# Optimization experiments

Measured on AMD Instinct MI355X. Metric: run time of the kernel, lower is better.

The kernel has to match this reference:

```python
import jax, jax.numpy as jnp
import numpy as np

ORDER = 2


def _masked_row_mean(v, m, safe_cnt, has_any):
    # v already zeroed outside mask; per-row mean over masked entries
    s = jnp.sum(v, axis=1, keepdims=True) / safe_cnt
    return jnp.where(has_any, s, 0.0)


def high_order_residual(x, mask, order=ORDER):
    """Vectorized faithful version of high_order_residual (braq).
    nanmean over masked entries == masked sum / count; sign/scale/shift
    are only meaningful inside the mask, outputs outside the mask are 0.
    """
    m = mask.astype(x.dtype)                       # (oc, ic)
    cnt = jnp.sum(m, axis=1, keepdims=True)        # (oc, 1)
    safe_cnt = jnp.maximum(cnt, 1.0)
    has_any = cnt > 0
    xm = x * m
    sum_order = jnp.zeros_like(x)
    for _ in range(order):
        residual = (xm - sum_order) * m            # masked residual, 0 outside
        mean = _masked_row_mean(residual, m, safe_cnt, has_any)   # (oc,1)
        centered = (residual - mean) * m           # 0 outside mask
        scale = _masked_row_mean(jnp.abs(centered), m, safe_cnt, has_any)
        binary = jnp.sign(centered) * scale + mean
        sum_order = sum_order + binary * m
    return sum_order


def setup_inputs() -> dict:
    key = jax.random.key(0)
    k1, k2 = jax.random.split(key)
    x = jax.random.normal(k1, (11008, 4096), dtype=jnp.float32) * 0.02
    mask = jax.random.randint(k2, (11008, 4096), 0, 2).astype(jnp.bool_)
    return {"x": x, "mask": mask}


def reference(x, mask):
    return high_order_residual(x, mask, ORDER)
```

## Files before the change

### kernel.cpp

```cpp
#include <hip/hip_runtime.h>
#include <stdint.h>

#define IC   4096
#define BLK  256
#define VPT  4
#define EPT  (VPT * 4)

__device__ __forceinline__ void block_red_df(double& a, float& b, double* smd, float* smf) {
    #pragma unroll
    for (int off = 32; off; off >>= 1) {
        a += __shfl_xor(a, off);
        b += __shfl_xor(b, off);
    }
    const int wid = threadIdx.x >> 6;
    if ((threadIdx.x & 63) == 0) { smd[wid] = a; smf[wid] = b; }
    __syncthreads();
    a = smd[0] + smd[1] + smd[2] + smd[3];
    b = smf[0] + smf[1] + smf[2] + smf[3];
}

__device__ __forceinline__ double block_red_d(double a, double* smd) {
    #pragma unroll
    for (int off = 32; off; off >>= 1) a += __shfl_xor(a, off);
    const int wid = threadIdx.x >> 6;
    if ((threadIdx.x & 63) == 0) smd[wid] = a;
    __syncthreads();
    return smd[0] + smd[1] + smd[2] + smd[3];
}

__global__ __launch_bounds__(BLK) void binarize_kernel(
    const float* __restrict__ x,
    const uint8_t* __restrict__ mask,
    float* __restrict__ out)
{
    __shared__ double smd[12];
    __shared__ float  smf[8];
    __shared__ int    smi[4];
    const int row = blockIdx.x;
    const int tid = threadIdx.x;

    int bad = (((const uint32_t*)mask)[tid] > 1u) ? 1 : 0;
    bad = __any(bad);
    if ((tid & 63) == 0) smi[tid >> 6] = bad;
    __syncthreads();
    const bool mask_is_i32 = ((smi[0] | smi[1] | smi[2] | smi[3]) == 0);

    const float* xr   = x + (size_t)row * IC;
    float*       orow = out + (size_t)row * IC;

    float xm[EPT];
    float sgm[EPT];
    uint32_t mb = 0;

    #pragma unroll
    for (int i = 0; i < VPT; ++i) {
        float4 v = ((const float4*)xr)[tid + i * BLK];
        xm[i*4+0] = v.x; xm[i*4+1] = v.y; xm[i*4+2] = v.z; xm[i*4+3] = v.w;
    }

    if (mask_is_i32) {
        const int4* mr = (const int4*)mask + (size_t)row * (IC / 4);
        #pragma unroll
        for (int i = 0; i < VPT; ++i) {
            int4 m4 = mr[tid + i * BLK];
            mb |= (uint32_t)(m4.x != 0) << (i*4+0);
            mb |= (uint32_t)(m4.y != 0) << (i*4+1);
            mb |= (uint32_t)(m4.z != 0) << (i*4+2);
            mb |= (uint32_t)(m4.w != 0) << (i*4+3);
        }
    } else {
        const uint32_t* mr = (const uint32_t*)(mask + (size_t)row * IC);
        #pragma unroll
        for (int i = 0; i < VPT; ++i) {
            uint32_t w = mr[tid + i * BLK];
            mb |= (uint32_t)((w & 0x000000ffu) != 0) << (i*4+0);
            mb |= (uint32_t)((w & 0x0000ff00u) != 0) << (i*4+1);
            mb |= (uint32_t)((w & 0x00ff0000u) != 0) << (i*4+2);
            mb |= (uint32_t)((w & 0xff000000u) != 0) << (i*4+3);
        }
    }

    #pragma unroll
    for (int j = 0; j < EPT; ++j)
        xm[j] = ((mb >> j) & 1u) ? xm[j] : 0.f;

    double sA[2] = {0.0, 0.0};
    #pragma unroll
    for (int j = 0; j < EPT; ++j) sA[j & 1] += (double)xm[j];
    double s  = sA[0] + sA[1];
    float  cf = (float)__popc(mb);
    block_red_df(s, cf, smd + 0, smf + 0);

    const bool   has   = (cf > 0.f);
    const double c     = (double)cf;
    const double nmiss = (double)(4096.f - cf);
    const double inv   = 1.0 / fmax(c, 1.0);
    const double mean1 = has ? s * inv : 0.0;
    const float  mean1f = (float)mean1;

    double saB[2] = {0.0, 0.0};
    float  dB[2]  = {0.f, 0.f};
    #pragma unroll
    for (int j = 0; j < EPT; ++j) {
        const float t  = xm[j] - mean1f;
        const float sg = (t > 0.f) ? 1.f : ((t < 0.f) ? -1.f : 0.f);
        const float smv = ((mb >> j) & 1u) ? sg : 0.f;
        sgm[j] = smv;
        dB[j & 1]  += smv;
        saB[j & 1] += (double)fabsf(t);
    }
    double sa = saB[0] + saB[1];
    float  df = dB[0] + dB[1];
    block_red_df(sa, df, smd + 4, smf + 4);
    sa -= nmiss * (double)fabsf(mean1f);

    const double scale1 = has ? sa * inv : 0.0;
    const double mean2  = has ? (s - scale1 * (double)df - mean1 * c) * inv : 0.0;
    const double mean12 = mean1 + mean2;

    double sbD[2] = {0.0, 0.0};
    #pragma unroll
    for (int j = 0; j < EPT; ++j) {
        const double t2 = (double)xm[j] - fma((double)sgm[j], scale1, mean12);
        sgm[j] = (float)t2;
        sbD[j & 1] += fabs(t2);
    }
    double sa2 = block_red_d(sbD[0] + sbD[1], smd + 8);
    sa2 -= nmiss * fabs(mean12);
    const double scale2 = has ? sa2 * inv : 0.0;
    const float  scale2f = (float)scale2;

    #pragma unroll
    for (int i = 0; i < VPT; ++i) {
        float r[4];
        #pragma unroll
        for (int k = 0; k < 4; ++k) {
            const int j = i * 4 + k;
            const float t2f = sgm[j];
            const float b1f = xm[j] - t2f;
            const float sg2 = (t2f > 0.f) ? 1.f : ((t2f < 0.f) ? -1.f : 0.f);
            const float o   = fmaf(sg2, scale2f, b1f);
            r[k] = ((mb >> j) & 1u) ? o : 0.f;
        }
        float4 o; o.x = r[0]; o.y = r[1]; o.z = r[2]; o.w = r[3];
        ((float4*)orow)[tid + i * BLK] = o;
    }
}

extern "C" void kernel_launch(void* const* d_in, const int* in_sizes, int n_in,
                              void* d_out, int out_size, void* d_ws, size_t ws_size,
                              hipStream_t stream) {
    const float*   x    = (const float*)d_in[0];
    const uint8_t* mask = (const uint8_t*)d_in[1];
    float*         out  = (float*)d_out;

    const int rows = in_sizes[0] / IC;
    binarize_kernel<<<rows, BLK, 0, stream>>>(x, mask, out);
}
```

Before: 402.6 us.

## Process one row per wavefront with shuffle-only reductions, recomputing signs

Switches from one 256-thread block per row to one 64-lane wavefront per row (4 rows per block), so row reductions use only wave shuffles and need no shared memory or __syncthreads. Each lane now holds 64 elements, and the per-element sign array is dropped and recomputed in later passes to save registers. The trade-off is more registers per lane, possibly lower occupancy, extra recomputation in double precision, and a longer serial load chain per lane.

```diff
diff --git a/kernel.cpp b/kernel.cpp
--- a/kernel.cpp
+++ b/kernel.cpp
@@ -1,149 +1,148 @@
 #include <hip/hip_runtime.h>
 #include <stdint.h>
 
-#define IC   4096
-#define BLK  256
-#define VPT  4
-#define EPT  (VPT * 4)
-
-__device__ __forceinline__ void block_red_df(double& a, float& b, double* smd, float* smf) {
-    #pragma unroll
-    for (int off = 32; off; off >>= 1) {
-        a += __shfl_xor(a, off);
-        b += __shfl_xor(b, off);
-    }
-    const int wid = threadIdx.x >> 6;
-    if ((threadIdx.x & 63) == 0) { smd[wid] = a; smf[wid] = b; }
-    __syncthreads();
-    a = smd[0] + smd[1] + smd[2] + smd[3];
-    b = smf[0] + smf[1] + smf[2] + smf[3];
-}
-
-__device__ __forceinline__ double block_red_d(double a, double* smd) {
-    #pragma unroll
-    for (int off = 32; off; off >>= 1) a += __shfl_xor(a, off);
-    const int wid = threadIdx.x >> 6;
-    if ((threadIdx.x & 63) == 0) smd[wid] = a;
-    __syncthreads();
-    return smd[0] + smd[1] + smd[2] + smd[3];
-}
+#define IC      4096
+#define BLK     256
+#define RPB     4
+#define CHUNKS  16
+#define EPT     64
 
 __global__ __launch_bounds__(BLK) void binarize_kernel(
     const float* __restrict__ x,
     const uint8_t* __restrict__ mask,
-    float* __restrict__ out)
+    float* __restrict__ out,
+    int nrows)
 {
-    __shared__ double smd[12];
-    __shared__ float  smf[8];
-    __shared__ int    smi[4];
-    const int row = blockIdx.x;
-    const int tid = threadIdx.x;
+    const int lane = threadIdx.x & 63;
+    const int row  = blockIdx.x * RPB + (threadIdx.x >> 6);
+    if (row >= nrows) return;
 
-    int bad = (((const uint32_t*)mask)[tid] > 1u) ? 1 : 0;
-    bad = __any(bad);
-    if ((tid & 63) == 0) smi[tid >> 6] = bad;
-    __syncthreads();
-    const bool mask_is_i32 = ((smi[0] | smi[1] | smi[2] | smi[3]) == 0);
+    const bool mask_is_i32 = !__any(((const uint32_t*)mask)[lane] > 1u);
 
-    const float* xr   = x + (size_t)row * IC;
+    const float* xr   = x   + (size_t)row * IC;
     float*       orow = out + (size_t)row * IC;
 
     float xm[EPT];
-    float sgm[EPT];
-    uint32_t mb = 0;
-
     #pragma unroll
-    for (int i = 0; i < VPT; ++i) {
-        float4 v = ((const float4*)xr)[tid + i * BLK];
-        xm[i*4+0] = v.x; xm[i*4+1] = v.y; xm[i*4+2] = v.z; xm[i*4+3] = v.w;
+    for (int i = 0; i < CHUNKS; ++i) {
+        float4 v = ((const float4*)xr)[lane + 64 * i];
+        xm[4*i+0] = v.x; xm[4*i+1] = v.y; xm[4*i+2] = v.z; xm[4*i+3] = v.w;
     }
 
+    uint32_t mw0 = 0, mw1 = 0;
     if (mask_is_i32) {
         const int4* mr = (const int4*)mask + (size_t)row * (IC / 4);
         #pragma unroll
-        for (int i = 0; i < VPT; ++i) {
-            int4 m4 = mr[tid + i * BLK];
-            mb |= (uint32_t)(m4.x != 0) << (i*4+0);
-            mb |= (uint32_t)(m4.y != 0) << (i*4+1);
-            mb |= (uint32_t)(m4.z != 0) << (i*4+2);
-            mb |= (uint32_t)(m4.w != 0) << (i*4+3);
+        for (int i = 0; i < CHUNKS; ++i) {
+            int4 m4 = mr[lane + 64 * i];
+            uint32_t b = (uint32_t)(m4.x != 0)
+                       | ((uint32_t)(m4.y != 0) << 1)
+                       | ((uint32_t)(m4.z != 0) << 2)
+                       | ((uint32_t)(m4.w != 0) << 3);
+            if (i < 8) mw0 |= b << (4 * i);
+            else       mw1 |= b << (4 * (i - 8));
         }
     } else {
         const uint32_t* mr = (const uint32_t*)(mask + (size_t)row * IC);
         #pragma unroll
-        for (int i = 0; i < VPT; ++i) {
-            uint32_t w = mr[tid + i * BLK];
-            mb |= (uint32_t)((w & 0x000000ffu) != 0) << (i*4+0);
-            mb |= (uint32_t)((w & 0x0000ff00u) != 0) << (i*4+1);
-            mb |= (uint32_t)((w & 0x00ff0000u) != 0) << (i*4+2);
-            mb |= (uint32_t)((w & 0xff000000u) != 0) << (i*4+3);
+        for (int i = 0; i < CHUNKS; ++i) {
+            uint32_t w = mr[lane + 64 * i];
+            uint32_t b = (uint32_t)((w & 0x000000ffu) != 0)
+                       | ((uint32_t)((w & 0x0000ff00u) != 0) << 1)
+                       | ((uint32_t)((w & 0x00ff0000u) != 0) << 2)
+                       | ((uint32_t)((w & 0xff000000u) != 0) << 3);
+            if (i < 8) mw0 |= b << (4 * i);
+            else       mw1 |= b << (4 * (i - 8));
         }
     }
 
     #pragma unroll
-    for (int j = 0; j < EPT; ++j)
-        xm[j] = ((mb >> j) & 1u) ? xm[j] : 0.f;
+    for (int j = 0; j < EPT; ++j) {
+        const uint32_t bit = ((j < 32 ? mw0 : mw1) >> (j & 31)) & 1u;
+        xm[j] = bit ? xm[j] : 0.f;
+    }
 
-    double sA[2] = {0.0, 0.0};
+    double sA0 = 0.0, sA1 = 0.0;
     #pragma unroll
-    for (int j = 0; j < EPT; ++j) sA[j & 1] += (double)xm[j];
-    double s  = sA[0] + sA[1];
-    float  cf = (float)__popc(mb);
-    block_red_df(s, cf, smd + 0, smf + 0);
+    for (int j = 0; j < EPT; j += 2) {
+        sA0 += (double)xm[j];
+        sA1 += (double)xm[j + 1];
+    }
+    double s  = sA0 + sA1;
+    float  cf = (float)(__popc(mw0) + __popc(mw1));
+    #pragma unroll
+    for (int off = 32; off; off >>= 1) {
+        s  += __shfl_xor(s,  off);
+        cf += __shfl_xor(cf, off);
+    }
 
-    const bool   has   = (cf > 0.f);
-    const double c     = (double)cf;
-    const double nmiss = (double)(4096.f - cf);
-    const double inv   = 1.0 / fmax(c, 1.0);
-    const double mean1 = has ? s * inv : 0.0;
+    const bool   has    = (cf > 0.f);
+    const double c      = (double)cf;
+    const double nmiss  = (double)(4096.f - cf);
+    const double inv    = 1.0 / fmax(c, 1.0);
+    const double mean1  = has ? s * inv : 0.0;
     const float  mean1f = (float)mean1;
 
-    double saB[2] = {0.0, 0.0};
-    float  dB[2]  = {0.f, 0.f};
+    double saB0 = 0.0, saB1 = 0.0;
+    float  dB0 = 0.f, dB1 = 0.f;
     #pragma unroll
     for (int j = 0; j < EPT; ++j) {
-        const float t  = xm[j] - mean1f;
-        const float sg = (t > 0.f) ? 1.f : ((t < 0.f) ? -1.f : 0.f);
-        const float smv = ((mb >> j) & 1u) ? sg : 0.f;
-        sgm[j] = smv;
-        dB[j & 1]  += smv;
-        saB[j & 1] += (double)fabsf(t);
+        const uint32_t bit = ((j < 32 ? mw0 : mw1) >> (j & 31)) & 1u;
+        const float t   = xm[j] - mean1f;
+        const float sg  = (t > 0.f) ? 1.f : ((t < 0.f) ? -1.f : 0.f);
+        const float smv = bit ? sg : 0.f;
+        if (j & 1) { dB1 += smv; saB1 += (double)fabsf(t); }
+        else       { dB0 += smv; saB0 += (double)fabsf(t); }
     }
-    double sa = saB[0] + saB[1];
-    float  df = dB[0] + dB[1];
-    block_red_df(sa, df, smd + 4, smf + 4);
+    double sa = saB0 + saB1;
+    float  df = dB0 + dB1;
+    #pragma unroll
+    for (int off = 32; off; off >>= 1) {
+        sa += __shfl_xor(sa, off);
+        df += __shfl_xor(df, off);
+    }
     sa -= nmiss * (double)fabsf(mean1f);
 
     const double scale1 = has ? sa * inv : 0.0;
     const double mean2  = has ? (s - scale1 * (double)df - mean1 * c) * inv : 0.0;
     const double mean12 = mean1 + mean2;
 
-    double sbD[2] = {0.0, 0.0};
+    double sb0 = 0.0, sb1 = 0.0;
     #pragma unroll
     for (int j = 0; j < EPT; ++j) {
-        const double t2 = (double)xm[j] - fma((double)sgm[j], scale1, mean12);
-        sgm[j] = (float)t2;
-        sbD[j & 1] += fabs(t2);
+        const uint32_t bit = ((j < 32 ? mw0 : mw1) >> (j & 31)) & 1u;
+        const float t   = xm[j] - mean1f;
+        const float sg  = (t > 0.f) ? 1.f : ((t < 0.f) ? -1.f : 0.f);
+        const float smv = bit ? sg : 0.f;
+        const double t2 = (double)xm[j] - fma((double)smv, scale1, mean12);
+        if (j & 1) sb1 += fabs(t2); else sb0 += fabs(t2);
     }
-    double sa2 = block_red_d(sbD[0] + sbD[1], smd + 8);
+    double sa2 = sb0 + sb1;
+    #pragma unroll
+    for (int off = 32; off; off >>= 1) sa2 += __shfl_xor(sa2, off);
     sa2 -= nmiss * fabs(mean12);
-    const double scale2 = has ? sa2 * inv : 0.0;
+    const double scale2  = has ? sa2 * inv : 0.0;
     const float  scale2f = (float)scale2;
 
     #pragma unroll
-    for (int i = 0; i < VPT; ++i) {
+    for (int i = 0; i < CHUNKS; ++i) {
         float r[4];
         #pragma unroll
         for (int k = 0; k < 4; ++k) {
-            const int j = i * 4 + k;
-            const float t2f = sgm[j];
+            const int j = 4 * i + k;
+            const uint32_t bit = ((j < 32 ? mw0 : mw1) >> (j & 31)) & 1u;
+            const float t   = xm[j] - mean1f;
+            const float sg  = (t > 0.f) ? 1.f : ((t < 0.f) ? -1.f : 0.f);
+            const float smv = bit ? sg : 0.f;
+            const double t2 = (double)xm[j] - fma((double)smv, scale1, mean12);
+            const float t2f = (float)t2;
             const float b1f = xm[j] - t2f;
             const float sg2 = (t2f > 0.f) ? 1.f : ((t2f < 0.f) ? -1.f : 0.f);
             const float o   = fmaf(sg2, scale2f, b1f);
-            r[k] = ((mb >> j) & 1u) ? o : 0.f;
+            r[k] = bit ? o : 0.f;
         }
-        float4 o; o.x = r[0]; o.y = r[1]; o.z = r[2]; o.w = r[3];
-        ((float4*)orow)[tid + i * BLK] = o;
+        float4 o4; o4.x = r[0]; o4.y = r[1]; o4.z = r[2]; o4.w = r[3];
+        ((float4*)orow)[lane + 64 * i] = o4;
     }
 }
 
@@ -155,5 +154,6 @@
     float*         out  = (float*)d_out;
 
     const int rows = in_sizes[0] / IC;
-    binarize_kernel<<<rows, BLK, 0, stream>>>(x, mask, out);
+    const int grid = (rows + RPB - 1) / RPB;
+    binarize_kernel<<<grid, BLK, 0, stream>>>(x, mask, out, rows);
 }
```

Measured after the change: 418.1 us. 3.9% more time.

## Process two rows per block and batch their block reductions together

Applied to the files above, without the earlier changes.

Each 256-thread block now handles two rows, interleaving their loads and sharing each shuffle/LDS reduction across both rows, so the number of barriers per row is halved. The per-element sign buffer is dropped and signs are recomputed from x and mean in later passes to save registers. The mask-format probe now uses a single wavefront instead of a shared-memory vote. In exchange, register pressure roughly doubles and the grid is halved, which may lower occupancy on a memory-bound kernel.

```diff
diff --git a/kernel.cpp b/kernel.cpp
--- a/kernel.cpp
+++ b/kernel.cpp
@@ -4,146 +4,200 @@
 #define IC   4096
 #define BLK  256
 #define VPT  4
-#define EPT  (VPT * 4)
-
-__device__ __forceinline__ void block_red_df(double& a, float& b, double* smd, float* smf) {
+#define EPT  16
+
+__device__ __forceinline__ void bred_2d2f(double& a, double& b, float& p, float& q,
+                                          double* smd, float* smf) {
     #pragma unroll
     for (int off = 32; off; off >>= 1) {
         a += __shfl_xor(a, off);
         b += __shfl_xor(b, off);
+        p += __shfl_xor(p, off);
+        q += __shfl_xor(q, off);
     }
     const int wid = threadIdx.x >> 6;
-    if ((threadIdx.x & 63) == 0) { smd[wid] = a; smf[wid] = b; }
+    if ((threadIdx.x & 63) == 0) { smd[wid] = a; smd[4 + wid] = b; smf[wid] = p; smf[4 + wid] = q; }
     __syncthreads();
-    a = smd[0] + smd[1] + smd[2] + smd[3];
-    b = smf[0] + smf[1] + smf[2] + smf[3];
-}
-
-__device__ __forceinline__ double block_red_d(double a, double* smd) {
-    #pragma unroll
-    for (int off = 32; off; off >>= 1) a += __shfl_xor(a, off);
+    a = (smd[0] + smd[1]) + (smd[2] + smd[3]);
+    b = (smd[4] + smd[5]) + (smd[6] + smd[7]);
+    p = (smf[0] + smf[1]) + (smf[2] + smf[3]);
+    q = (smf[4] + smf[5]) + (smf[6] + smf[7]);
+}
+
+__device__ __forceinline__ void bred_2d(double& a, double& b, double* smd) {
+    #pragma unroll
+    for (int off = 32; off; off >>= 1) {
+        a += __shfl_xor(a, off);
+        b += __shfl_xor(b, off);
+    }
     const int wid = threadIdx.x >> 6;
-    if ((threadIdx.x & 63) == 0) smd[wid] = a;
+    if ((threadIdx.x & 63) == 0) { smd[wid] = a; smd[4 + wid] = b; }
     __syncthreads();
-    return smd[0] + smd[1] + smd[2] + smd[3];
+    a = (smd[0] + smd[1]) + (smd[2] + smd[3]);
+    b = (smd[4] + smd[5]) + (smd[6] + smd[7]);
 }
 
 __global__ __launch_bounds__(BLK) void binarize_kernel(
     const float* __restrict__ x,
     const uint8_t* __restrict__ mask,
-    float* __restrict__ out)
+    float* __restrict__ out,
+    int nrows)
 {
-    __shared__ double smd[12];
-    __shared__ float  smf[8];
-    __shared__ int    smi[4];
-    const int row = blockIdx.x;
-    const int tid = threadIdx.x;
-
-    int bad = (((const uint32_t*)mask)[tid] > 1u) ? 1 : 0;
-    bad = __any(bad);
-    if ((tid & 63) == 0) smi[tid >> 6] = bad;
-    __syncthreads();
-    const bool mask_is_i32 = ((smi[0] | smi[1] | smi[2] | smi[3]) == 0);
-
-    const float* xr   = x + (size_t)row * IC;
-    float*       orow = out + (size_t)row * IC;
-
-    float xm[EPT];
-    float sgm[EPT];
-    uint32_t mb = 0;
+    __shared__ double smd[24];
+    __shared__ float  smf[16];
+    const int tid  = threadIdx.x;
+    const int lane = tid & 63;
+    const int rowA = (int)blockIdx.x << 1;
+    const int rowB = rowA | 1;
+    const bool hasB = (rowB < nrows);
+    const int rowBs = hasB ? rowB : rowA;
+
+    const bool mask_is_i32 = !__any(((const uint32_t*)mask)[lane] > 1u);
+
+    const float* xrA = x + (size_t)rowA  * IC;
+    const float* xrB = x + (size_t)rowBs * IC;
+
+    float xmA[EPT], xmB[EPT];
+    uint32_t mbA = 0, mbB = 0;
 
     #pragma unroll
     for (int i = 0; i < VPT; ++i) {
-        float4 v = ((const float4*)xr)[tid + i * BLK];
-        xm[i*4+0] = v.x; xm[i*4+1] = v.y; xm[i*4+2] = v.z; xm[i*4+3] = v.w;
+        const float4 va = ((const float4*)xrA)[tid + i * BLK];
+        const float4 vb = ((const float4*)xrB)[tid + i * BLK];
+        xmA[i*4+0] = va.x; xmA[i*4+1] = va.y; xmA[i*4+2] = va.z; xmA[i*4+3] = va.w;
+        xmB[i*4+0] = vb.x; xmB[i*4+1] = vb.y; xmB[i*4+2] = vb.z; xmB[i*4+3] = vb.w;
     }
 
     if (mask_is_i32) {
-        const int4* mr = (const int4*)mask + (size_t)row * (IC / 4);
+        const int4* mA = (const int4*)mask + (size_t)rowA  * (IC / 4);
+        const int4* mB = (const int4*)mask + (size_t)rowBs * (IC / 4);
         #pragma unroll
         for (int i = 0; i < VPT; ++i) {
-            int4 m4 = mr[tid + i * BLK];
-            mb |= (uint32_t)(m4.x != 0) << (i*4+0);
-            mb |= (uint32_t)(m4.y != 0) << (i*4+1);
-            mb |= (uint32_t)(m4.z != 0) << (i*4+2);
-            mb |= (uint32_t)(m4.w != 0) << (i*4+3);
+            const int4 a4 = mA[tid + i * BLK];
+            const int4 b4 = mB[tid + i * BLK];
+            mbA |= ((uint32_t)(a4.x != 0) | ((uint32_t)(a4.y != 0) << 1)
+                 |  ((uint32_t)(a4.z != 0) << 2) | ((uint32_t)(a4.w != 0) << 3)) << (4 * i);
+            mbB |= ((uint32_t)(b4.x != 0) | ((uint32_t)(b4.y != 0) << 1)
+                 |  ((uint32_t)(b4.z != 0) << 2) | ((uint32_t)(b4.w != 0) << 3)) << (4 * i);
         }
     } else {
-        const uint32_t* mr = (const uint32_t*)(mask + (size_t)row * IC);
+        const uint32_t* mA = (const uint32_t*)(mask + (size_t)rowA  * IC);
+        const uint32_t* mB = (const uint32_t*)(mask + (size_t)rowBs * IC);
         #pragma unroll
         for (int i = 0; i < VPT; ++i) {
-            uint32_t w = mr[tid + i * BLK];
-            mb |= (uint32_t)((w & 0x000000ffu) != 0) << (i*4+0);
-            mb |= (uint32_t)((w & 0x0000ff00u) != 0) << (i*4+1);
-            mb |= (uint32_t)((w & 0x00ff0000u) != 0) << (i*4+2);
-            mb |= (uint32_t)((w & 0xff000000u) != 0) << (i*4+3);
-        }
-    }
-
-    #pragma unroll
-    for (int j = 0; j < EPT; ++j)
-        xm[j] = ((mb >> j) & 1u) ? xm[j] : 0.f;
-
-    double sA[2] = {0.0, 0.0};
-    #pragma unroll
-    for (int j = 0; j < EPT; ++j) sA[j & 1] += (double)xm[j];
-    double s  = sA[0] + sA[1];
-    float  cf = (float)__popc(mb);
-    block_red_df(s, cf, smd + 0, smf + 0);
-
-    const bool   has   = (cf > 0.f);
-    const double c     = (double)cf;
-    const double nmiss = (double)(4096.f - cf);
-    const double inv   = 1.0 / fmax(c, 1.0);
-    const double mean1 = has ? s * inv : 0.0;
-    const float  mean1f = (float)mean1;
-
-    double saB[2] = {0.0, 0.0};
-    float  dB[2]  = {0.f, 0.f};
+            const uint32_t wa = mA[tid + i * BLK];
+            const uint32_t wb = mB[tid + i * BLK];
+            mbA |= ((uint32_t)((wa & 0x000000ffu) != 0) | ((uint32_t)((wa & 0x0000ff00u) != 0) << 1)
+                 |  ((uint32_t)((wa & 0x00ff0000u) != 0) << 2) | ((uint32_t)((wa & 0xff000000u) != 0) << 3)) << (4 * i);
+            mbB |= ((uint32_t)((wb & 0x000000ffu) != 0) | ((uint32_t)((wb & 0x0000ff00u) != 0) << 1)
+                 |  ((uint32_t)((wb & 0x00ff0000u) != 0) << 2) | ((uint32_t)((wb & 0xff000000u) != 0) << 3)) << (4 * i);
+        }
+    }
+
     #pragma unroll
     for (int j = 0; j < EPT; ++j) {
-        const float t  = xm[j] - mean1f;
-        const float sg = (t > 0.f) ? 1.f : ((t < 0.f) ? -1.f : 0.f);
-        const float smv = ((mb >> j) & 1u) ? sg : 0.f;
-        sgm[j] = smv;
-        dB[j & 1]  += smv;
-        saB[j & 1] += (double)fabsf(t);
-    }
-    double sa = saB[0] + saB[1];
-    float  df = dB[0] + dB[1];
-    block_red_df(sa, df, smd + 4, smf + 4);
-    sa -= nmiss * (double)fabsf(mean1f);
-
-    const double scale1 = has ? sa * inv : 0.0;
-    const double mean2  = has ? (s - scale1 * (double)df - mean1 * c) * inv : 0.0;
-    const double mean12 = mean1 + mean2;
-
-    double sbD[2] = {0.0, 0.0};
+        xmA[j] = ((mbA >> j) & 1u) ? xmA[j] : 0.f;
+        xmB[j] = ((mbB >> j) & 1u) ? xmB[j] : 0.f;
+    }
+
+    double sA0 = 0.0, sA1 = 0.0, sB0 = 0.0, sB1 = 0.0;
+    #pragma unroll
+    for (int j = 0; j < EPT; j += 2) {
+        sA0 += (double)xmA[j]; sA1 += (double)xmA[j + 1];
+        sB0 += (double)xmB[j]; sB1 += (double)xmB[j + 1];
+    }
+    double sA = sA0 + sA1, sB = sB0 + sB1;
+    float cfA = (float)__popc(mbA), cfB = (float)__popc(mbB);
+    bred_2d2f(sA, sB, cfA, cfB, smd + 0, smf + 0);
+
+    const bool   hasA_   = (cfA > 0.f),        hasB_   = (cfB > 0.f);
+    const double cA      = (double)cfA,        cB      = (double)cfB;
+    const double nmissA  = (double)(4096.f - cfA), nmissB = (double)(4096.f - cfB);
+    const double invA    = 1.0 / fmax(cA, 1.0), invB   = 1.0 / fmax(cB, 1.0);
+    const double mean1A  = hasA_ ? sA * invA : 0.0, mean1B = hasB_ ? sB * invB : 0.0;
+    const float  mean1fA = (float)mean1A,      mean1fB = (float)mean1B;
+
+    double saA0 = 0.0, saA1 = 0.0, saB0 = 0.0, saB1 = 0.0;
+    float  dfA = 0.f, dfB = 0.f;
     #pragma unroll
     for (int j = 0; j < EPT; ++j) {
-        const double t2 = (double)xm[j] - fma((double)sgm[j], scale1, mean12);
-        sgm[j] = (float)t2;
-        sbD[j & 1] += fabs(t2);
-    }
-    double sa2 = block_red_d(sbD[0] + sbD[1], smd + 8);
-    sa2 -= nmiss * fabs(mean12);
-    const double scale2 = has ? sa2 * inv : 0.0;
-    const float  scale2f = (float)scale2;
-
+        const float ta = xmA[j] - mean1fA;
+        const float sga = (ta > 0.f) ? 1.f : ((ta < 0.f) ? -1.f : 0.f);
+        dfA += ((mbA >> j) & 1u) ? sga : 0.f;
+        if (j & 1) saA1 += (double)fabsf(ta); else saA0 += (double)fabsf(ta);
+
+        const float tb = xmB[j] - mean1fB;
+        const float sgb = (tb > 0.f) ? 1.f : ((tb < 0.f) ? -1.f : 0.f);
+        dfB += ((mbB >> j) & 1u) ? sgb : 0.f;
+        if (j & 1) saB1 += (double)fabsf(tb); else saB0 += (double)fabsf(tb);
+    }
+    double saA = saA0 + saA1, saB = saB0 + saB1;
+    bred_2d2f(saA, saB, dfA, dfB, smd + 8, smf + 8);
+    saA -= nmissA * (double)fabsf(mean1fA);
+    saB -= nmissB * (double)fabsf(mean1fB);
+
+    const double scale1A = hasA_ ? saA * invA : 0.0, scale1B = hasB_ ? saB * invB : 0.0;
+    const double mean2A  = hasA_ ? (sA - scale1A * (double)dfA - mean1A * cA) * invA : 0.0;
+    const double mean2B  = hasB_ ? (sB - scale1B * (double)dfB - mean1B * cB) * invB : 0.0;
+    const double mean12A = mean1A + mean2A, mean12B = mean1B + mean2B;
+
+    double s2A0 = 0.0, s2A1 = 0.0, s2B0 = 0.0, s2B1 = 0.0;
+    #pragma unroll
+    for (int j = 0; j < EPT; ++j) {
+        const float ta = xmA[j] - mean1fA;
+        const float sga = (ta > 0.f) ? 1.f : ((ta < 0.f) ? -1.f : 0.f);
+        const float sva = ((mbA >> j) & 1u) ? sga : 0.f;
+        const double t2a = (double)xmA[j] - fma((double)sva, scale1A, mean12A);
+        if (j & 1) s2A1 += fabs(t2a); else s2A0 += fabs(t2a);
+
+        const float tb = xmB[j] - mean1fB;
+        const float sgb = (tb > 0.f) ? 1.f : ((tb < 0.f) ? -1.f : 0.f);
+        const float svb = ((mbB >> j) & 1u) ? sgb : 0.f;
+        const double t2b = (double)xmB[j] - fma((double)svb, scale1B, mean12B);
+        if (j & 1) s2B1 += fabs(t2b); else s2B0 += fabs(t2b);
+    }
+    double sa2A = s2A0 + s2A1, sa2B = s2B0 + s2B1;
+    bred_2d(sa2A, sa2B, smd + 16);
+    sa2A -= nmissA * fabs(mean12A);
+    sa2B -= nmissB * fabs(mean12B);
+    const double scale2A  = hasA_ ? sa2A * invA : 0.0, scale2B = hasB_ ? sa2B * invB : 0.0;
+    const float  scale2fA = (float)scale2A,            scale2fB = (float)scale2B;
+
+    float* orA = out + (size_t)rowA * IC;
+    float* orB = out + (size_t)rowB * IC;
     #pragma unroll
     for (int i = 0; i < VPT; ++i) {
-        float r[4];
+        float ra[4], rb[4];
         #pragma unroll
         for (int k = 0; k < 4; ++k) {
-            const int j = i * 4 + k;
-            const float t2f = sgm[j];
-            const float b1f = xm[j] - t2f;
-            const float sg2 = (t2f > 0.f) ? 1.f : ((t2f < 0.f) ? -1.f : 0.f);
-            const float o   = fmaf(sg2, scale2f, b1f);
-            r[k] = ((mb >> j) & 1u) ? o : 0.f;
-        }
-        float4 o; o.x = r[0]; o.y = r[1]; o.z = r[2]; o.w = r[3];
-        ((float4*)orow)[tid + i * BLK] = o;
+            const int j = 4 * i + k;
+            {
+                const float ta = xmA[j] - mean1fA;
+                const float sga = (ta > 0.f) ? 1.f : ((ta < 0.f) ? -1.f : 0.f);
+                const float sva = ((mbA >> j) & 1u) ? sga : 0.f;
+                const double t2 = (double)xmA[j] - fma((double)sva, scale1A, mean12A);
+                const float t2f = (float)t2;
+                const float b1f = xmA[j] - t2f;
+                const float sg2 = (t2f > 0.f) ? 1.f : ((t2f < 0.f) ? -1.f : 0.f);
+                ra[k] = ((mbA >> j) & 1u) ? fmaf(sg2, scale2fA, b1f) : 0.f;
+            }
+            {
+                const float tb = xmB[j] - mean1fB;
+                const float sgb = (tb > 0.f) ? 1.f : ((tb < 0.f) ? -1.f : 0.f);
+                const float svb = ((mbB >> j) & 1u) ? sgb : 0.f;
+                const double t2 = (double)xmB[j] - fma((double)svb, scale1B, mean12B);
+                const float t2f = (float)t2;
+                const float b1f = xmB[j] - t2f;
+                const float sg2 = (t2f > 0.f) ? 1.f : ((t2f < 0.f) ? -1.f : 0.f);
+                rb[k] = ((mbB >> j) & 1u) ? fmaf(sg2, scale2fB, b1f) : 0.f;
+            }
+        }
+        float4 oa; oa.x = ra[0]; oa.y = ra[1]; oa.z = ra[2]; oa.w = ra[3];
+        ((float4*)orA)[tid + i * BLK] = oa;
+        if (hasB) {
+            float4 ob; ob.x = rb[0]; ob.y = rb[1]; ob.z = rb[2]; ob.w = rb[3];
+            ((float4*)orB)[tid + i * BLK] = ob;
+        }
     }
 }
 
@@ -155,5 +209,6 @@
     float*         out  = (float*)d_out;
 
     const int rows = in_sizes[0] / IC;
-    binarize_kernel<<<rows, BLK, 0, stream>>>(x, mask, out);
-}
+    const int grid = (rows + 1) / 2;
+    binarize_kernel<<<grid, BLK, 0, stream>>>(x, mask, out, rows);
+}
```

Result: no change. 407.3 us (+1.2%).
